# Kernel tuning notes

Hardware: AMD Instinct MI355X
Metric: run time of the kernel (lower is better)

Reference implementation:

```python
import jax, jax.numpy as jnp
import numpy as np

B, S, H = 32, 2048, 1024

def setup_inputs() -> dict:
    key = jax.random.key(0)
    k1, k2, k3, k4, k5 = jax.random.split(key, 5)
    hidden = jax.random.normal(k1, (1, B, H), dtype=jnp.float32)
    encoder_outputs = jax.random.normal(k2, (B, S, H), dtype=jnp.float32)
    # nn.Linear(2H, H): weight [H, 2H], bias [H]
    W_attn = jax.random.normal(k3, (H, 2 * H), dtype=jnp.float32) * (1.0 / np.sqrt(2 * H))
    b_attn = jax.random.normal(k4, (H,), dtype=jnp.float32) * 0.01
    # nn.Linear(H, 1, bias=False): weight [1, H] -> stored as [H]
    v = jax.random.normal(k5, (H,), dtype=jnp.float32) * (1.0 / np.sqrt(H))
    return {"hidden": hidden, "encoder_outputs": encoder_outputs,
            "W_attn": W_attn, "b_attn": b_attn, "v": v}

def reference(hidden, encoder_outputs, W_attn, b_attn, v):
    # hidden: [1, B, H] -> [B, H]; encoder_outputs: [B, S, H]
    h = hidden[0]  # [B, H]
    # cat((hidden_repeated, enc), -1) @ W_attn.T == h @ Wh.T + enc @ We.T
    Wh = W_attn[:, :H]   # [H, H] acts on hidden part
    We = W_attn[:, H:]   # [H, H] acts on encoder part
    h_proj = jnp.einsum('bh,oh->bo', h, Wh)                    # [B, H]
    e_proj = jnp.einsum('bsh,oh->bso', encoder_outputs, We)    # [B, S, H]
    energy = jnp.tanh(e_proj + h_proj[:, None, :] + b_attn)    # [B, S, H]
    attention = jnp.einsum('bsh,h->bs', energy, v)             # [B, S]
    return jax.nn.softmax(attention, axis=1)
```

## Files before the change

### kernel.cpp

```cpp
#include <hip/hip_runtime.h>
#include <hip/hip_bf16.h>
#include <cstdint>


#define HDIM 1024
#define SDIM 2048
#define MTOT 65536

typedef __attribute__((ext_vector_type(8))) short short8;
typedef __attribute__((ext_vector_type(4))) float floatx4;

__device__ __forceinline__ unsigned short f2bf(float f) {
    unsigned int u = __float_as_uint(f);
    u += 0x7fffu + ((u >> 16) & 1u);
    return (unsigned short)(u >> 16);
}
__device__ __forceinline__ unsigned int pack2(float a, float b) {
    return (unsigned int)f2bf(a) | ((unsigned int)f2bf(b) << 16);
}
__device__ __forceinline__ float fast_tanh(float x) {
    float e2 = __expf(2.f * x);
    return 1.f - 2.f * __builtin_amdgcn_rcpf(e2 + 1.f);
}

__global__ __launch_bounds__(256) void convert_W2(const float* __restrict__ W,
                                                  unsigned short* __restrict__ Wbf2) {
    int T = blockIdx.x * 256 + threadIdx.x;
    int n  = T >> 7;
    int k8 = T & 127;
    int k  = k8 * 8;
    const float4* src = (const float4*)(W + (size_t)n * 2048 + 1024 + k);
    float4 f0 = src[0], f1 = src[1];
    int jt = n >> 4, lc = n & 15, kc = k8 >> 2, g = k8 & 3;
    uint4 u;
    u.x = pack2(f0.x, f0.y); u.y = pack2(f0.z, f0.w);
    u.z = pack2(f1.x, f1.y); u.w = pack2(f1.z, f1.w);
    *(uint4*)(Wbf2 + (size_t)(jt * 32 + kc) * 512 + (g * 16 + lc) * 8) = u;
}

__global__ __launch_bounds__(256) void calc_c(const float* __restrict__ hid,
                                              const float* __restrict__ W,
                                              const float* __restrict__ bias,
                                              float* __restrict__ c) {
    __shared__ float red[4][32];
    const int o = blockIdx.x;
    const int wave = threadIdx.x >> 6, lane = threadIdx.x & 63;
    const int k = wave * 256 + lane * 4;
    const float4 wv = *(const float4*)(W + (size_t)o * 2048 + k);
    float acc[32];
#pragma unroll
    for (int b = 0; b < 32; ++b) {
        const float4 h = *(const float4*)(hid + b * HDIM + k);
        acc[b] = wv.x * h.x + wv.y * h.y + wv.z * h.z + wv.w * h.w;
    }
#pragma unroll
    for (int b = 0; b < 32; ++b) {
        float x = acc[b];
        for (int off = 32; off; off >>= 1) x += __shfl_xor(x, off);
        if (lane == 0) red[wave][b] = x;
    }
    __syncthreads();
    if (threadIdx.x < 32) {
        int b = threadIdx.x;
        c[b * HDIM + o] = red[0][b] + red[1][b] + red[2][b] + red[3][b] + bias[o];
    }
}

#define PHN 8
#define PHK 128

__global__ __launch_bounds__(512, 2) void attn_fused(const float* __restrict__ enc,
                                                     const unsigned short* __restrict__ Wbf2,
                                                     const float* __restrict__ c,
                                                     const float* __restrict__ v,
                                                     float* __restrict__ part) {
    __shared__ __align__(16) unsigned short slab[2][64 * 128];

    const int tid  = threadIdx.x;
    const int lane = tid & 63;
    const int wave = tid >> 6;
    const int grp  = lane >> 4;
    const int lc   = lane & 15;

    const int m0 = blockIdx.x * 64;
    const int b  = m0 >> 11;

    const int s_kk   = (lane & 31) * 4;
    const int s_rsub = lane >> 5;
    const int s_c16  = (lane & 31) >> 1;
    const int s_b8   = lane & 1;

    floatx4 acc[2][4][4];
#pragma unroll
    for (int cg = 0; cg < 2; ++cg)
#pragma unroll
        for (int i = 0; i < 4; ++i)
#pragma unroll
            for (int j = 0; j < 4; ++j) acc[cg][i][j] = (floatx4){0.f, 0.f, 0.f, 0.f};

    const short8* Bfr = (const short8*)Wbf2;

    float4 ld[4];
#pragma unroll
    for (int q = 0; q < 4; ++q) {
        int row = wave * 8 + q * 2 + s_rsub;
        ld[q] = *(const float4*)(enc + (size_t)(m0 + row) * HDIM + s_kk);
    }
#pragma unroll
    for (int q = 0; q < 4; ++q) {
        int row  = wave * 8 + q * 2 + s_rsub;
        int slot = s_c16 ^ (row & 7);
        uint2 u = {pack2(ld[q].x, ld[q].y), pack2(ld[q].z, ld[q].w)};
        *(uint2*)(&slab[0][row * 128 + slot * 8 + s_b8 * 4]) = u;
    }

    short8 bf[4], bn[4];
#pragma unroll
    for (int j = 0; j < 4; ++j)
        bf[j] = Bfr[(size_t)((wave * 8 + 0 * 4 + j) * 32 + 0) * 64 + lane];

#pragma unroll 1
    for (int p = 0; p < PHN; ++p) {
        __syncthreads();

        if (p < PHN - 1) {
#pragma unroll
            for (int q = 0; q < 4; ++q) {
                int row = wave * 8 + q * 2 + s_rsub;
                ld[q] = *(const float4*)(enc + (size_t)(m0 + row) * HDIM +
                                         (p + 1) * PHK + s_kk);
            }
        }

        const unsigned short* sl = slab[p & 1];
#pragma unroll
        for (int s = 0; s < 8; ++s) {
            const int cg = s >> 2, kc = s & 3;
            short8 af[4];
#pragma unroll
            for (int i = 0; i < 4; ++i) {
                int row  = i * 16 + lc;
                int slot = (kc * 4 + grp) ^ (lc & 7);
                af[i] = *(const short8*)(sl + row * 128 + slot * 16 / 2);
            }
            {
                const int cg2 = (s < 7) ? ((s + 1) >> 2) : 0;
                const int kc2 = (s < 7) ? ((s + 1) & 3) : 0;
                const int pn  = (s < 7) ? p : ((p < PHN - 1) ? p + 1 : p);
#pragma unroll
                for (int j = 0; j < 4; ++j)
                    bn[j] = Bfr[(size_t)((wave * 8 + cg2 * 4 + j) * 32 +
                                         pn * 4 + kc2) * 64 + lane];
            }
#pragma unroll
            for (int i = 0; i < 4; ++i)
#pragma unroll
                for (int j = 0; j < 4; ++j)
                    acc[cg][i][j] = __builtin_amdgcn_mfma_f32_16x16x32_bf16(
                        af[i], bf[j], acc[cg][i][j], 0, 0, 0);
#pragma unroll
            for (int j = 0; j < 4; ++j) bf[j] = bn[j];
        }

        if (p < PHN - 1) {
#pragma unroll
            for (int q = 0; q < 4; ++q) {
                int row  = wave * 8 + q * 2 + s_rsub;
                int slot = s_c16 ^ (row & 7);
                uint2 u = {pack2(ld[q].x, ld[q].y), pack2(ld[q].z, ld[q].w)};
                *(uint2*)(&slab[(p + 1) & 1][row * 128 + slot * 8 + s_b8 * 4]) = u;
            }
        }
    }

    float rowsum[4][4];
#pragma unroll
    for (int i = 0; i < 4; ++i)
#pragma unroll
        for (int r = 0; r < 4; ++r) rowsum[i][r] = 0.f;

#pragma unroll
    for (int cg = 0; cg < 2; ++cg)
#pragma unroll
        for (int j = 0; j < 4; ++j) {
            const int n  = wave * 128 + cg * 64 + j * 16 + lc;
            const float vn = v[n];
            const float cv = c[b * HDIM + n];
#pragma unroll
            for (int i = 0; i < 4; ++i)
#pragma unroll
                for (int r = 0; r < 4; ++r)
                    rowsum[i][r] = fmaf(fast_tanh(acc[cg][i][j][r] + cv), vn,
                                        rowsum[i][r]);
        }

#pragma unroll
    for (int i = 0; i < 4; ++i)
#pragma unroll
        for (int r = 0; r < 4; ++r) {
            float x = rowsum[i][r];
            x += __shfl_xor(x, 8);
            x += __shfl_xor(x, 4);
            x += __shfl_xor(x, 2);
            x += __shfl_xor(x, 1);
            if (lc == 0)
                part[(size_t)wave * MTOT + m0 + i * 16 + grp * 4 + r] = x;
        }
}

__global__ __launch_bounds__(256) void softmax_k(const float* __restrict__ partials,
                                                 float* __restrict__ out, int npart) {
    __shared__ float wred[4];
    const int bb = blockIdx.x;
    const int tid = threadIdx.x;
    const int wave = tid >> 6, lane = tid & 63;

    float vals[8];
    float lmax = -INFINITY;
#pragma unroll
    for (int q = 0; q < 8; ++q) {
        const size_t idx = (size_t)bb * SDIM + q * 256 + tid;
        float x = 0.f;
        for (int p = 0; p < npart; ++p) x += partials[(size_t)p * MTOT + idx];
        vals[q] = x;
        lmax = fmaxf(lmax, x);
    }
    for (int off = 32; off; off >>= 1) lmax = fmaxf(lmax, __shfl_xor(lmax, off));
    if (lane == 0) wred[wave] = lmax;
    __syncthreads();
    lmax = fmaxf(fmaxf(wred[0], wred[1]), fmaxf(wred[2], wred[3]));
    __syncthreads();

    float e[8];
    float s = 0.f;
#pragma unroll
    for (int q = 0; q < 8; ++q) {
        e[q] = __expf(vals[q] - lmax);
        s += e[q];
    }
    for (int off = 32; off; off >>= 1) s += __shfl_xor(s, off);
    if (lane == 0) wred[wave] = s;
    __syncthreads();
    s = wred[0] + wred[1] + wred[2] + wred[3];
    const float inv = 1.f / s;
#pragma unroll
    for (int q = 0; q < 8; ++q)
        out[(size_t)bb * SDIM + q * 256 + tid] = e[q] * inv;
}

extern "C" void kernel_launch(void* const* d_in, const int* in_sizes, int n_in,
                              void* d_out, int out_size, void* d_ws, size_t ws_size,
                              hipStream_t stream) {
    const float* hidden = (const float*)d_in[0];
    const float* enc    = (const float*)d_in[1];
    const float* W      = (const float*)d_in[2];
    const float* battn  = (const float*)d_in[3];
    const float* v      = (const float*)d_in[4];
    float* out = (float*)d_out;

    char* ws = (char*)d_ws;
    float* c             = (float*)ws;
    float* part          = (float*)(ws + (128 << 10));
    unsigned short* Wbf2 = (unsigned short*)(ws + (128 << 10) + (2 << 20));

    hipLaunchKernelGGL(convert_W2, dim3(512),  dim3(256), 0, stream, W, Wbf2);
    hipLaunchKernelGGL(calc_c,     dim3(1024), dim3(256), 0, stream, hidden, W, battn, c);
    hipLaunchKernelGGL(attn_fused, dim3(1024), dim3(512), 0, stream, enc, Wbf2, c, v, part);
    hipLaunchKernelGGL(softmax_k,  dim3(32),   dim3(256), 0, stream, part, out, 8);
}
```

Before: 540.4 us.

## Merge prep kernels, reduce wave partials in-block, interleave slab stores, set MFMA priority

Merges the weight-conversion and hidden-projection kernels into one launch, which saves a kernel launch. The attention kernel now sums its per-wave partial logits through shared memory before writing, so softmax reads one logit per row instead of eight partials. The bf16 slab stores are spread across the last four MFMA steps rather than issued after the loop. MFMA issue is wrapped in s_setprio to favour matrix work. Reusing slab as the reduction buffer adds a block-wide barrier at the end of the attention kernel.

New measurement: 521.7 us. 1.04x faster.

```diff
diff --git a/kernel.cpp b/kernel.cpp
--- a/kernel.cpp
+++ b/kernel.cpp
@@ -23,46 +23,46 @@
     return 1.f - 2.f * __builtin_amdgcn_rcpf(e2 + 1.f);
 }
 
-__global__ __launch_bounds__(256) void convert_W2(const float* __restrict__ W,
-                                                  unsigned short* __restrict__ Wbf2) {
-    int T = blockIdx.x * 256 + threadIdx.x;
-    int n  = T >> 7;
-    int k8 = T & 127;
-    int k  = k8 * 8;
-    const float4* src = (const float4*)(W + (size_t)n * 2048 + 1024 + k);
-    float4 f0 = src[0], f1 = src[1];
-    int jt = n >> 4, lc = n & 15, kc = k8 >> 2, g = k8 & 3;
-    uint4 u;
-    u.x = pack2(f0.x, f0.y); u.y = pack2(f0.z, f0.w);
-    u.z = pack2(f1.x, f1.y); u.w = pack2(f1.z, f1.w);
-    *(uint4*)(Wbf2 + (size_t)(jt * 32 + kc) * 512 + (g * 16 + lc) * 8) = u;
-}
-
-__global__ __launch_bounds__(256) void calc_c(const float* __restrict__ hid,
-                                              const float* __restrict__ W,
-                                              const float* __restrict__ bias,
-                                              float* __restrict__ c) {
+__global__ __launch_bounds__(256) void prep(const float* __restrict__ W,
+                                            unsigned short* __restrict__ Wbf2,
+                                            const float* __restrict__ hid,
+                                            const float* __restrict__ bias,
+                                            float* __restrict__ c) {
     __shared__ float red[4][32];
-    const int o = blockIdx.x;
-    const int wave = threadIdx.x >> 6, lane = threadIdx.x & 63;
-    const int k = wave * 256 + lane * 4;
-    const float4 wv = *(const float4*)(W + (size_t)o * 2048 + k);
-    float acc[32];
-#pragma unroll
-    for (int b = 0; b < 32; ++b) {
-        const float4 h = *(const float4*)(hid + b * HDIM + k);
-        acc[b] = wv.x * h.x + wv.y * h.y + wv.z * h.z + wv.w * h.w;
-    }
-#pragma unroll
-    for (int b = 0; b < 32; ++b) {
-        float x = acc[b];
-        for (int off = 32; off; off >>= 1) x += __shfl_xor(x, off);
-        if (lane == 0) red[wave][b] = x;
-    }
-    __syncthreads();
-    if (threadIdx.x < 32) {
-        int b = threadIdx.x;
-        c[b * HDIM + o] = red[0][b] + red[1][b] + red[2][b] + red[3][b] + bias[o];
+    if (blockIdx.x < 512) {
+        int T = blockIdx.x * 256 + threadIdx.x;
+        int n  = T >> 7;
+        int k8 = T & 127;
+        int k  = k8 * 8;
+        const float4* src = (const float4*)(W + (size_t)n * 2048 + 1024 + k);
+        float4 f0 = src[0], f1 = src[1];
+        int jt = n >> 4, lc = n & 15, kc = k8 >> 2, g = k8 & 3;
+        uint4 u;
+        u.x = pack2(f0.x, f0.y); u.y = pack2(f0.z, f0.w);
+        u.z = pack2(f1.x, f1.y); u.w = pack2(f1.z, f1.w);
+        *(uint4*)(Wbf2 + (size_t)(jt * 32 + kc) * 512 + (g * 16 + lc) * 8) = u;
+    } else {
+        const int o = blockIdx.x - 512;
+        const int wave = threadIdx.x >> 6, lane = threadIdx.x & 63;
+        const int k = wave * 256 + lane * 4;
+        const float4 wv = *(const float4*)(W + (size_t)o * 2048 + k);
+        float acc[32];
+#pragma unroll
+        for (int b = 0; b < 32; ++b) {
+            const float4 h = *(const float4*)(hid + b * HDIM + k);
+            acc[b] = wv.x * h.x + wv.y * h.y + wv.z * h.z + wv.w * h.w;
+        }
+#pragma unroll
+        for (int b = 0; b < 32; ++b) {
+            float x = acc[b];
+            for (int off = 32; off; off >>= 1) x += __shfl_xor(x, off);
+            if (lane == 0) red[wave][b] = x;
+        }
+        __syncthreads();
+        if (threadIdx.x < 32) {
+            int b = threadIdx.x;
+            c[b * HDIM + o] = red[0][b] + red[1][b] + red[2][b] + red[3][b] + bias[o];
+        }
     }
 }
 
@@ -73,7 +73,7 @@
                                                      const unsigned short* __restrict__ Wbf2,
                                                      const float* __restrict__ c,
                                                      const float* __restrict__ v,
-                                                     float* __restrict__ part) {
+                                                     float* __restrict__ logits) {
     __shared__ __align__(16) unsigned short slab[2][64 * 128];
 
     const int tid  = threadIdx.x;
@@ -152,24 +152,23 @@
                     bn[j] = Bfr[(size_t)((wave * 8 + cg2 * 4 + j) * 32 +
                                          pn * 4 + kc2) * 64 + lane];
             }
+            __builtin_amdgcn_s_setprio(1);
 #pragma unroll
             for (int i = 0; i < 4; ++i)
 #pragma unroll
                 for (int j = 0; j < 4; ++j)
                     acc[cg][i][j] = __builtin_amdgcn_mfma_f32_16x16x32_bf16(
                         af[i], bf[j], acc[cg][i][j], 0, 0, 0);
-#pragma unroll
-            for (int j = 0; j < 4; ++j) bf[j] = bn[j];
-        }
-
-        if (p < PHN - 1) {
-#pragma unroll
-            for (int q = 0; q < 4; ++q) {
+            __builtin_amdgcn_s_setprio(0);
+            if (p < PHN - 1 && s >= 4) {
+                const int q = s - 4;
                 int row  = wave * 8 + q * 2 + s_rsub;
                 int slot = s_c16 ^ (row & 7);
                 uint2 u = {pack2(ld[q].x, ld[q].y), pack2(ld[q].z, ld[q].w)};
                 *(uint2*)(&slab[(p + 1) & 1][row * 128 + slot * 8 + s_b8 * 4]) = u;
             }
+#pragma unroll
+            for (int j = 0; j < 4; ++j) bf[j] = bn[j];
         }
     }
 
@@ -194,6 +193,7 @@
                                         rowsum[i][r]);
         }
 
+    float* red = (float*)slab;
 #pragma unroll
     for (int i = 0; i < 4; ++i)
 #pragma unroll
@@ -203,13 +203,19 @@
             x += __shfl_xor(x, 4);
             x += __shfl_xor(x, 2);
             x += __shfl_xor(x, 1);
-            if (lc == 0)
-                part[(size_t)wave * MTOT + m0 + i * 16 + grp * 4 + r] = x;
-        }
-}
-
-__global__ __launch_bounds__(256) void softmax_k(const float* __restrict__ partials,
-                                                 float* __restrict__ out, int npart) {
+            if (lc == 0) red[wave * 64 + i * 16 + grp * 4 + r] = x;
+        }
+    __syncthreads();
+    if (tid < 64) {
+        float ssum = 0.f;
+#pragma unroll
+        for (int w = 0; w < 8; ++w) ssum += red[w * 64 + tid];
+        logits[m0 + tid] = ssum;
+    }
+}
+
+__global__ __launch_bounds__(256) void softmax_k(const float* __restrict__ logits,
+                                                 float* __restrict__ out) {
     __shared__ float wred[4];
     const int bb = blockIdx.x;
     const int tid = threadIdx.x;
@@ -219,11 +225,8 @@
     float lmax = -INFINITY;
 #pragma unroll
     for (int q = 0; q < 8; ++q) {
-        const size_t idx = (size_t)bb * SDIM + q * 256 + tid;
-        float x = 0.f;
-        for (int p = 0; p < npart; ++p) x += partials[(size_t)p * MTOT + idx];
-        vals[q] = x;
-        lmax = fmaxf(lmax, x);
+        vals[q] = logits[(size_t)bb * SDIM + q * 256 + tid];
+        lmax = fmaxf(lmax, vals[q]);
     }
     for (int off = 32; off; off >>= 1) lmax = fmaxf(lmax, __shfl_xor(lmax, off));
     if (lane == 0) wred[wave] = lmax;
@@ -260,11 +263,10 @@
 
     char* ws = (char*)d_ws;
     float* c             = (float*)ws;
-    float* part          = (float*)(ws + (128 << 10));
-    unsigned short* Wbf2 = (unsigned short*)(ws + (128 << 10) + (2 << 20));
-
-    hipLaunchKernelGGL(convert_W2, dim3(512),  dim3(256), 0, stream, W, Wbf2);
-    hipLaunchKernelGGL(calc_c,     dim3(1024), dim3(256), 0, stream, hidden, W, battn, c);
-    hipLaunchKernelGGL(attn_fused, dim3(1024), dim3(512), 0, stream, enc, Wbf2, c, v, part);
-    hipLaunchKernelGGL(softmax_k,  dim3(32),   dim3(256), 0, stream, part, out, 8);
-}
+    float* logits        = (float*)(ws + (128 << 10));
+    unsigned short* Wbf2 = (unsigned short*)(ws + (384 << 10));
+
+    hipLaunchKernelGGL(prep,       dim3(1536), dim3(256), 0, stream, W, Wbf2, hidden, battn, c);
+    hipLaunchKernelGGL(attn_fused, dim3(1024), dim3(512), 0, stream, enc, Wbf2, c, v, logits);
+    hipLaunchKernelGGL(softmax_k,  dim3(32),   dim3(256), 0, stream, logits, out);
+}
```
